# Performance work log

Hardware: AMD Instinct MI355X
Metric: run time of the kernel (lower is better)

Reference implementation:

```python
import jax, jax.numpy as jnp
import numpy as np

N_NODES = 50000
N_EDGES = 800000
D = 64        # in_channels == out_channels
EDGE_DIM = 32
H = 8         # num_heads
HD = D // H   # head_dim


def _layer_norm(x, g, b, eps=1e-5):
    m = jnp.mean(x, axis=-1, keepdims=True)
    v = jnp.mean((x - m) ** 2, axis=-1, keepdims=True)
    return (x - m) * jax.lax.rsqrt(v + eps) * g + b


def setup_inputs() -> dict:
    key = jax.random.key(0)
    ks = jax.random.split(key, 20)
    s = 0.05
    inp = {
        'x': jax.random.normal(ks[0], (N_NODES, D), jnp.float32),
        'edge_index': jax.random.randint(ks[1], (2, N_EDGES), 0, N_NODES, dtype=jnp.int64),
        'edge_attr': jax.random.normal(ks[2], (N_EDGES, EDGE_DIM), jnp.float32),
        'Wq': jax.random.normal(ks[3], (D, D), jnp.float32) * s,
        'bq': jnp.zeros((D,), jnp.float32),
        'Wk': jax.random.normal(ks[4], (D, D), jnp.float32) * s,
        'bk': jnp.zeros((D,), jnp.float32),
        'Wv': jax.random.normal(ks[5], (D, D), jnp.float32) * s,
        'bv': jnp.zeros((D,), jnp.float32),
        'We': jax.random.normal(ks[6], (EDGE_DIM, D), jnp.float32) * s,
        'be': jnp.zeros((D,), jnp.float32),
        'Wo': jax.random.normal(ks[7], (D, D), jnp.float32) * s,
        'bo': jnp.zeros((D,), jnp.float32),
        'g1': jnp.ones((D,), jnp.float32),
        'b1': jnp.zeros((D,), jnp.float32),
        'g2': jnp.ones((D,), jnp.float32),
        'b2': jnp.zeros((D,), jnp.float32),
        'Wf1': jax.random.normal(ks[8], (D, 2 * D), jnp.float32) * s,
        'bf1': jnp.zeros((2 * D,), jnp.float32),
        'Wf2': jax.random.normal(ks[9], (2 * D, D), jnp.float32) * s,
        'bf2': jnp.zeros((D,), jnp.float32),
    }
    return inp


def reference(x, edge_index, edge_attr, Wq, bq, Wk, bk, Wv, bv, We, be, Wo, bo,
              g1, b1, g2, b2, Wf1, bf1, Wf2, bf2):
    num_nodes = x.shape[0]
    # add_self_loops with fill_value=0.0
    ar = jnp.arange(num_nodes, dtype=edge_index.dtype)
    src = jnp.concatenate([edge_index[0], ar])
    dst = jnp.concatenate([edge_index[1], ar])
    ea = jnp.concatenate([edge_attr, jnp.zeros((num_nodes, edge_attr.shape[1]), edge_attr.dtype)])

    q = (x @ Wq + bq).reshape(num_nodes, H, HD)
    k = (x @ Wk + bk).reshape(num_nodes, H, HD)
    v = (x @ Wv + bv).reshape(num_nodes, H, HD)
    ee = (ea @ We + be).reshape(-1, H, HD)  # [E', H, HD]

    # gather, score, global softmax over all edges (dim=0, as in source)
    scores = jnp.sum(q[dst] * (k[src] + ee), axis=-1) / (HD ** 0.5)  # [E', H]
    alpha = jax.nn.softmax(scores, axis=0)
    messages = alpha[..., None] * (v[src] + ee)  # [E', H, HD]

    out_sum = jax.ops.segment_sum(messages, dst, num_segments=num_nodes)
    counts = jax.ops.segment_sum(jnp.ones(dst.shape, x.dtype), dst, num_segments=num_nodes)
    counts = jnp.maximum(counts, 1.0)
    out = (out_sum / counts[:, None, None]).reshape(num_nodes, -1)

    h = _layer_norm(x + out @ Wo + bo, g1, b1)
    ffn = jax.nn.gelu(h @ Wf1 + bf1, approximate=False) @ Wf2 + bf2
    # dropout in eval mode -> identity
    return _layer_norm(h + ffn, g2, b2)
```

## Files before the change

kernel.cpp:

```cpp
#include <hip/hip_runtime.h>
#include <hip/hip_bf16.h>
#include <math.h>

#define N_NODES 50000
#define N_EDGES 800000
#define D 64
#define ED 32

#define Q_OFF    0
#define K_OFF    1600000
#define V_OFF    3200000
#define EE_OFF   4800000
#define OS_OFF   17600000
#define S_OFF    19200000
#define RP_OFF   19200016
#define SRCP_OFF 19250018
#define EIDP_OFF 20050018
#define DEG_OFF  20850018
#define WOFF_OFF 20900018
#define BSUM_OFF 20950018
#define H_OFF    0
#define F1_OFF   EE_OFF

typedef __bf16 bf16x8 __attribute__((ext_vector_type(8)));
typedef float  f32x4  __attribute__((ext_vector_type(4)));

__device__ __forceinline__ ushort f2bf(float f) {
  uint u = __float_as_uint(f);
  uint r = (u + 0x7FFFu + ((u >> 16) & 1u)) >> 16;
  return (ushort)r;
}
__device__ __forceinline__ float bfu2f(ushort u) {
  return __uint_as_float(((uint)u) << 16);
}
__device__ __forceinline__ void unpack8(uint4 u, float (&f)[8]) {
  f[0] = __uint_as_float(u.x << 16); f[1] = __uint_as_float(u.x & 0xffff0000u);
  f[2] = __uint_as_float(u.y << 16); f[3] = __uint_as_float(u.y & 0xffff0000u);
  f[4] = __uint_as_float(u.z << 16); f[5] = __uint_as_float(u.z & 0xffff0000u);
  f[6] = __uint_as_float(u.w << 16); f[7] = __uint_as_float(u.w & 0xffff0000u);
}
__device__ __forceinline__ bf16x8 pack_bf8(float4 a, float4 b) {
  bf16x8 r;
  r[0] = (__bf16)a.x; r[1] = (__bf16)a.y; r[2] = (__bf16)a.z; r[3] = (__bf16)a.w;
  r[4] = (__bf16)b.x; r[5] = (__bf16)b.y; r[6] = (__bf16)b.z; r[7] = (__bf16)b.w;
  return r;
}

__global__ __launch_bounds__(256) void k_qkv_mfma(
    const float* __restrict__ x,
    const float* __restrict__ Wq, const float* __restrict__ bq,
    const float* __restrict__ Wk, const float* __restrict__ bk,
    const float* __restrict__ Wv, const float* __restrict__ bv,
    ushort* __restrict__ q, ushort* __restrict__ k, ushort* __restrict__ v,
    int* __restrict__ deg, float* __restrict__ S) {
  const int tid0 = blockIdx.x * 256 + threadIdx.x;
  if (tid0 < N_NODES) deg[tid0] = 0;
  if (tid0 < 16) S[tid0] = 0.f;

  const int lane = threadIdx.x & 63;
  const int wid  = threadIdx.x >> 6;
  const int r  = lane & 15;
  const int kg = lane >> 4;
  const float* Ws[3] = {Wq, Wk, Wv};
  const float* bs[3] = {bq, bk, bv};
  ushort* os[3] = {q, k, v};

  bf16x8 afrag[3][4][2];
  float  bias[3][4][4];
#pragma unroll
  for (int m = 0; m < 3; ++m)
#pragma unroll
    for (int nt = 0; nt < 4; ++nt) {
#pragma unroll
      for (int kk = 0; kk < 2; ++kk)
#pragma unroll
        for (int j = 0; j < 8; ++j)
          afrag[m][nt][kk][j] = (__bf16)Ws[m][(kk * 32 + kg * 8 + j) * 64 + nt * 16 + r];
#pragma unroll
      for (int j = 0; j < 4; ++j) bias[m][nt][j] = bs[m][nt * 16 + kg * 4 + j];
    }

  const int ntile = N_NODES / 16;
  const int nw = gridDim.x * 4;
  for (int t = blockIdx.x * 4 + wid; t < ntile; t += nw) {
    const int base = t * 16;
    const float4* xr = reinterpret_cast<const float4*>(x + (size_t)(base + r) * 64 + kg * 8);
    const bf16x8 xf0 = pack_bf8(xr[0], xr[1]);
    const bf16x8 xf1 = pack_bf8(xr[8], xr[9]);
#pragma unroll
    for (int m = 0; m < 3; ++m) {
#pragma unroll
      for (int nt = 0; nt < 4; ++nt) {
        f32x4 acc = {bias[m][nt][0], bias[m][nt][1], bias[m][nt][2], bias[m][nt][3]};
        acc = __builtin_amdgcn_mfma_f32_16x16x32_bf16(afrag[m][nt][0], xf0, acc, 0, 0, 0);
        acc = __builtin_amdgcn_mfma_f32_16x16x32_bf16(afrag[m][nt][1], xf1, acc, 0, 0, 0);
        ushort4 pk;
        pk.x = f2bf(acc[0]); pk.y = f2bf(acc[1]); pk.z = f2bf(acc[2]); pk.w = f2bf(acc[3]);
        *reinterpret_cast<ushort4*>(os[m] + (size_t)(base + r) * 64 + nt * 16 + kg * 4) = pk;
      }
    }
  }
}

__global__ __launch_bounds__(256) void k_hist(const int* __restrict__ edst,
                                              int* __restrict__ deg) {
  const int i = blockIdx.x * 256 + threadIdx.x;
  if (i < N_EDGES) atomicAdd(&deg[edst[i]], 1);
}

__global__ __launch_bounds__(256) void k_scan_a(const int* __restrict__ deg,
                                                int* __restrict__ bsum) {
  __shared__ int lds[256];
  const int i = blockIdx.x * 256 + threadIdx.x;
  lds[threadIdx.x] = (i < N_NODES) ? deg[i] : 0;
  __syncthreads();
  for (int s = 128; s > 0; s >>= 1) {
    if (threadIdx.x < s) lds[threadIdx.x] += lds[threadIdx.x + s];
    __syncthreads();
  }
  if (threadIdx.x == 0) bsum[blockIdx.x] = lds[0];
}

__global__ __launch_bounds__(256) void k_scan_b(int* __restrict__ bsum, int nb) {
  __shared__ int lds[256];
  const int t = threadIdx.x;
  const int d = (t < nb) ? bsum[t] : 0;
  lds[t] = d;
  __syncthreads();
  for (int off = 1; off < 256; off <<= 1) {
    const int val = (t >= off) ? lds[t - off] : 0;
    __syncthreads();
    lds[t] += val;
    __syncthreads();
  }
  if (t < nb) bsum[t] = lds[t] - d;
}

__global__ __launch_bounds__(256) void k_scan_c(const int* __restrict__ deg,
                                                const int* __restrict__ bsum,
                                                int* __restrict__ rowptr,
                                                int* __restrict__ woff) {
  __shared__ int lds[256];
  const int i = blockIdx.x * 256 + threadIdx.x;
  const int d = (i < N_NODES) ? deg[i] : 0;
  lds[threadIdx.x] = d;
  __syncthreads();
  for (int off = 1; off < 256; off <<= 1) {
    const int val = (threadIdx.x >= off) ? lds[threadIdx.x - off] : 0;
    __syncthreads();
    lds[threadIdx.x] += val;
    __syncthreads();
  }
  const int ex = bsum[blockIdx.x] + lds[threadIdx.x] - d;
  if (i < N_NODES) { rowptr[i] = ex; woff[i] = ex; }
  if (i == N_NODES - 1) rowptr[N_NODES] = ex + d;
}

__global__ __launch_bounds__(256) void k_scatter(const int* __restrict__ esrc,
                                                 const int* __restrict__ edst,
                                                 int* __restrict__ woff,
                                                 int* __restrict__ srcp,
                                                 int* __restrict__ eidp) {
  const int i = blockIdx.x * 256 + threadIdx.x;
  if (i < N_EDGES) {
    const int pos = atomicAdd(&woff[edst[i]], 1);
    srcp[pos] = esrc[i];
    eidp[pos] = i;
  }
}

__global__ __launch_bounds__(256) void k_ee_mfma(
    const int* __restrict__ eidp, const float* __restrict__ ea,
    const float* __restrict__ We, const float* __restrict__ be,
    unsigned char* __restrict__ ee8) {
  const int lane = threadIdx.x & 63;
  const int wid  = threadIdx.x >> 6;
  const int r  = lane & 15;
  const int kg = lane >> 4;

  bf16x8 afrag[4];
  float  bias[4][4];
#pragma unroll
  for (int nt = 0; nt < 4; ++nt) {
#pragma unroll
    for (int j = 0; j < 8; ++j)
      afrag[nt][j] = (__bf16)We[(kg * 8 + j) * 64 + nt * 16 + r];
#pragma unroll
    for (int j = 0; j < 4; ++j) bias[nt][j] = be[nt * 16 + kg * 4 + j];
  }

  const int ntile = N_EDGES / 16;
  const int nw = gridDim.x * 4;
  for (int t = blockIdx.x * 4 + wid; t < ntile; t += nw) {
    const int base = t * 16;
    const int eid = eidp[base + r];
    const float4* ar = reinterpret_cast<const float4*>(ea + (size_t)eid * 32 + kg * 8);
    const bf16x8 bfrag = pack_bf8(ar[0], ar[1]);
#pragma unroll
    for (int nt = 0; nt < 4; ++nt) {
      f32x4 acc = {bias[nt][0], bias[nt][1], bias[nt][2], bias[nt][3]};
      acc = __builtin_amdgcn_mfma_f32_16x16x32_bf16(afrag[nt], bfrag, acc, 0, 0, 0);
      uint rr = (uint)__builtin_amdgcn_cvt_pk_fp8_f32(acc[0], acc[1], 0, false);
      rr = (uint)__builtin_amdgcn_cvt_pk_fp8_f32(acc[2], acc[3], (int)rr, true);
      *reinterpret_cast<uint*>(ee8 + (size_t)(base + r) * 64 + nt * 16 + kg * 4) = rr;
    }
  }
}

__global__ __launch_bounds__(256) void k_gather(
    const int* __restrict__ rowptr, const int* __restrict__ srcp,
    const unsigned char* __restrict__ ee8,
    const ushort* __restrict__ qb, const ushort* __restrict__ kb,
    const ushort* __restrict__ vb, const float* __restrict__ be,
    ushort* __restrict__ osum, float* __restrict__ S) {
  const int lane = threadIdx.x & 63;
  const int wid  = threadIdx.x >> 6;
  const int h = lane & 7, ei = lane >> 3;
  float bes[8];
#pragma unroll
  for (int i = 0; i < 8; ++i) bes[i] = be[h * 8 + i];
  float sacc = 0.f;
  const int nw = gridDim.x * 4;
  for (int n = blockIdx.x * 4 + wid; n < N_NODES; n += nw) {
    const int beg = rowptr[n], end = rowptr[n + 1];
    float qv[8];
    unpack8(*reinterpret_cast<const uint4*>(qb + (size_t)n * 64 + h * 8), qv);
    float macc[8];
#pragma unroll
    for (int i = 0; i < 8; ++i) macc[i] = 0.f;
    if (ei == 0) {
      float kv[8], vv[8];
      unpack8(*reinterpret_cast<const uint4*>(kb + (size_t)n * 64 + h * 8), kv);
      unpack8(*reinterpret_cast<const uint4*>(vb + (size_t)n * 64 + h * 8), vv);
      float sc = 0.f;
#pragma unroll
      for (int i = 0; i < 8; ++i) sc = fmaf(qv[i], kv[i] + bes[i], sc);
      const float w = __expf(sc * 0.3535533905932738f);
      sacc += w;
#pragma unroll
      for (int i = 0; i < 8; ++i) macc[i] = w * (vv[i] + bes[i]);
    }
    int p = beg + ei;
    int src = (p < end) ? srcp[p] : 0;
    for (; p < end; p += 8) {
      const int nsrc = (p + 8 < end) ? srcp[p + 8] : 0;
      float ev[8], kv[8], vv[8];
      const uint2 er8 = *reinterpret_cast<const uint2*>(ee8 + (size_t)p * 64 + h * 8);
      ev[0] = __builtin_amdgcn_cvt_f32_fp8((int)er8.x, 0);
      ev[1] = __builtin_amdgcn_cvt_f32_fp8((int)er8.x, 1);
      ev[2] = __builtin_amdgcn_cvt_f32_fp8((int)er8.x, 2);
      ev[3] = __builtin_amdgcn_cvt_f32_fp8((int)er8.x, 3);
      ev[4] = __builtin_amdgcn_cvt_f32_fp8((int)er8.y, 0);
      ev[5] = __builtin_amdgcn_cvt_f32_fp8((int)er8.y, 1);
      ev[6] = __builtin_amdgcn_cvt_f32_fp8((int)er8.y, 2);
      ev[7] = __builtin_amdgcn_cvt_f32_fp8((int)er8.y, 3);
      unpack8(*reinterpret_cast<const uint4*>(kb + (size_t)src * 64 + h * 8), kv);
      unpack8(*reinterpret_cast<const uint4*>(vb + (size_t)src * 64 + h * 8), vv);
      float sc = 0.f;
#pragma unroll
      for (int i = 0; i < 8; ++i) sc = fmaf(qv[i], kv[i] + ev[i], sc);
      const float w = __expf(sc * 0.3535533905932738f);
      sacc += w;
#pragma unroll
      for (int i = 0; i < 8; ++i) macc[i] = fmaf(w, vv[i] + ev[i], macc[i]);
      src = nsrc;
    }
#pragma unroll
    for (int i = 0; i < 8; ++i) {
      macc[i] += __shfl_xor(macc[i], 8);
      macc[i] += __shfl_xor(macc[i], 16);
      macc[i] += __shfl_xor(macc[i], 32);
    }
    if (ei == 0) {
      uint pk[4];
#pragma unroll
      for (int i = 0; i < 4; ++i)
        pk[i] = (uint)f2bf(macc[2 * i]) | ((uint)f2bf(macc[2 * i + 1]) << 16);
      *reinterpret_cast<uint4*>(osum + (size_t)n * 64 + h * 8) =
          make_uint4(pk[0], pk[1], pk[2], pk[3]);
    }
  }
  sacc += __shfl_xor(sacc, 8);
  sacc += __shfl_xor(sacc, 16);
  sacc += __shfl_xor(sacc, 32);
  if (ei == 0) atomicAdd(&S[h], sacc);
}

__global__ __launch_bounds__(256) void k_ln1_mfma(
    const ushort* __restrict__ osum, const int* __restrict__ rowptr,
    const float* __restrict__ S, const float* __restrict__ x,
    const float* __restrict__ Wo, const float* __restrict__ bo,
    const float* __restrict__ g1, const float* __restrict__ b1,
    ushort* __restrict__ h) {
  const int lane = threadIdx.x & 63;
  const int wid  = threadIdx.x >> 6;
  const int r  = lane & 15;
  const int kg = lane >> 4;

  bf16x8 afrag[4][2];
  float bias[4][4], g1f[4][4], b1f[4][4];
#pragma unroll
  for (int nt = 0; nt < 4; ++nt) {
#pragma unroll
    for (int kk = 0; kk < 2; ++kk)
#pragma unroll
      for (int j = 0; j < 8; ++j)
        afrag[nt][kk][j] = (__bf16)Wo[(kk * 32 + kg * 8 + j) * 64 + nt * 16 + r];
#pragma unroll
    for (int j = 0; j < 4; ++j) {
      bias[nt][j] = bo[nt * 16 + kg * 4 + j];
      g1f[nt][j]  = g1[nt * 16 + kg * 4 + j];
      b1f[nt][j]  = b1[nt * 16 + kg * 4 + j];
    }
  }
  float invSv[8];
#pragma unroll
  for (int i = 0; i < 8; ++i) invSv[i] = 1.0f / S[i];

  const int ntile = N_NODES / 16;
  const int nw = gridDim.x * 4;
  for (int t = blockIdx.x * 4 + wid; t < ntile; t += nw) {
    const int node = t * 16 + r;
    const float invc = 1.0f / (float)(rowptr[node + 1] - rowptr[node] + 1);
    bf16x8 bfrag[2];
#pragma unroll
    for (int kk = 0; kk < 2; ++kk) {
      float tmp[8];
      unpack8(*reinterpret_cast<const uint4*>(osum + (size_t)node * 64 + kk * 32 + kg * 8), tmp);
      const float sc = invSv[kk * 4 + kg] * invc;
      bf16x8 bf;
#pragma unroll
      for (int e = 0; e < 8; ++e) bf[e] = (__bf16)(tmp[e] * sc);
      bfrag[kk] = bf;
    }
    float tv[4][4];
    float sum = 0.f;
#pragma unroll
    for (int nt = 0; nt < 4; ++nt) {
      f32x4 acc = {bias[nt][0], bias[nt][1], bias[nt][2], bias[nt][3]};
      acc = __builtin_amdgcn_mfma_f32_16x16x32_bf16(afrag[nt][0], bfrag[0], acc, 0, 0, 0);
      acc = __builtin_amdgcn_mfma_f32_16x16x32_bf16(afrag[nt][1], bfrag[1], acc, 0, 0, 0);
      const float4 xv = *reinterpret_cast<const float4*>(x + (size_t)node * 64 + nt * 16 + kg * 4);
      tv[nt][0] = acc[0] + xv.x; tv[nt][1] = acc[1] + xv.y;
      tv[nt][2] = acc[2] + xv.z; tv[nt][3] = acc[3] + xv.w;
      sum += (tv[nt][0] + tv[nt][1]) + (tv[nt][2] + tv[nt][3]);
    }
    sum += __shfl_xor(sum, 16);
    sum += __shfl_xor(sum, 32);
    const float m = sum * (1.0f / 64.0f);
    float var = 0.f;
#pragma unroll
    for (int nt = 0; nt < 4; ++nt)
#pragma unroll
      for (int j = 0; j < 4; ++j) { const float d = tv[nt][j] - m; var = fmaf(d, d, var); }
    var += __shfl_xor(var, 16);
    var += __shfl_xor(var, 32);
    const float rinv = rsqrtf(var * (1.0f / 64.0f) + 1e-5f);
#pragma unroll
    for (int nt = 0; nt < 4; ++nt) {
      ushort4 pk;
      pk.x = f2bf((tv[nt][0] - m) * rinv * g1f[nt][0] + b1f[nt][0]);
      pk.y = f2bf((tv[nt][1] - m) * rinv * g1f[nt][1] + b1f[nt][1]);
      pk.z = f2bf((tv[nt][2] - m) * rinv * g1f[nt][2] + b1f[nt][2]);
      pk.w = f2bf((tv[nt][3] - m) * rinv * g1f[nt][3] + b1f[nt][3]);
      *reinterpret_cast<ushort4*>(h + (size_t)node * 64 + nt * 16 + kg * 4) = pk;
    }
  }
}

__global__ __launch_bounds__(256) void k_ffn1_mfma(
    const ushort* __restrict__ h, const float* __restrict__ Wf1,
    const float* __restrict__ bf1, ushort* __restrict__ f1) {
  const int lane = threadIdx.x & 63;
  const int wid  = threadIdx.x >> 6;
  const int r  = lane & 15;
  const int kg = lane >> 4;

  bf16x8 afrag[8][2];
  float bias[8][4];
#pragma unroll
  for (int nt = 0; nt < 8; ++nt) {
#pragma unroll
    for (int kk = 0; kk < 2; ++kk)
#pragma unroll
      for (int j = 0; j < 8; ++j)
        afrag[nt][kk][j] = (__bf16)Wf1[(kk * 32 + kg * 8 + j) * 128 + nt * 16 + r];
#pragma unroll
    for (int j = 0; j < 4; ++j) bias[nt][j] = bf1[nt * 16 + kg * 4 + j];
  }

  const int ntile = N_NODES / 16;
  const int nw = gridDim.x * 4;
  for (int t = blockIdx.x * 4 + wid; t < ntile; t += nw) {
    const int node = t * 16 + r;
    const bf16x8 bf0 = *reinterpret_cast<const bf16x8*>(h + (size_t)node * 64 + kg * 8);
    const bf16x8 bf1g = *reinterpret_cast<const bf16x8*>(h + (size_t)node * 64 + 32 + kg * 8);
#pragma unroll
    for (int nt = 0; nt < 8; ++nt) {
      f32x4 acc = {bias[nt][0], bias[nt][1], bias[nt][2], bias[nt][3]};
      acc = __builtin_amdgcn_mfma_f32_16x16x32_bf16(afrag[nt][0], bf0, acc, 0, 0, 0);
      acc = __builtin_amdgcn_mfma_f32_16x16x32_bf16(afrag[nt][1], bf1g, acc, 0, 0, 0);
      ushort4 pk;
      pk.x = f2bf(0.5f * acc[0] * (1.0f + erff(acc[0] * 0.7071067811865475f)));
      pk.y = f2bf(0.5f * acc[1] * (1.0f + erff(acc[1] * 0.7071067811865475f)));
      pk.z = f2bf(0.5f * acc[2] * (1.0f + erff(acc[2] * 0.7071067811865475f)));
      pk.w = f2bf(0.5f * acc[3] * (1.0f + erff(acc[3] * 0.7071067811865475f)));
      *reinterpret_cast<ushort4*>(f1 + (size_t)node * 128 + nt * 16 + kg * 4) = pk;
    }
  }
}

__global__ __launch_bounds__(256) void k_ffn2_mfma(
    const ushort* __restrict__ f1, const ushort* __restrict__ h,
    const float* __restrict__ Wf2, const float* __restrict__ bf2,
    const float* __restrict__ g2, const float* __restrict__ b2,
    float* __restrict__ out) {
  const int lane = threadIdx.x & 63;
  const int wid  = threadIdx.x >> 6;
  const int r  = lane & 15;
  const int kg = lane >> 4;

  bf16x8 afrag[4][4];
  float bias[4][4], g2f[4][4], b2f[4][4];
#pragma unroll
  for (int nt = 0; nt < 4; ++nt) {
#pragma unroll
    for (int kk = 0; kk < 4; ++kk)
#pragma unroll
      for (int j = 0; j < 8; ++j)
        afrag[nt][kk][j] = (__bf16)Wf2[(kk * 32 + kg * 8 + j) * 64 + nt * 16 + r];
#pragma unroll
    for (int j = 0; j < 4; ++j) {
      bias[nt][j] = bf2[nt * 16 + kg * 4 + j];
      g2f[nt][j]  = g2[nt * 16 + kg * 4 + j];
      b2f[nt][j]  = b2[nt * 16 + kg * 4 + j];
    }
  }

  const int ntile = N_NODES / 16;
  const int nw = gridDim.x * 4;
  for (int t = blockIdx.x * 4 + wid; t < ntile; t += nw) {
    const int node = t * 16 + r;
    bf16x8 bfrag[4];
#pragma unroll
    for (int kk = 0; kk < 4; ++kk)
      bfrag[kk] = *reinterpret_cast<const bf16x8*>(f1 + (size_t)node * 128 + kk * 32 + kg * 8);
    float tv[4][4];
    float sum = 0.f;
#pragma unroll
    for (int nt = 0; nt < 4; ++nt) {
      f32x4 acc = {bias[nt][0], bias[nt][1], bias[nt][2], bias[nt][3]};
      acc = __builtin_amdgcn_mfma_f32_16x16x32_bf16(afrag[nt][0], bfrag[0], acc, 0, 0, 0);
      acc = __builtin_amdgcn_mfma_f32_16x16x32_bf16(afrag[nt][1], bfrag[1], acc, 0, 0, 0);
      acc = __builtin_amdgcn_mfma_f32_16x16x32_bf16(afrag[nt][2], bfrag[2], acc, 0, 0, 0);
      acc = __builtin_amdgcn_mfma_f32_16x16x32_bf16(afrag[nt][3], bfrag[3], acc, 0, 0, 0);
      const ushort4 hv = *reinterpret_cast<const ushort4*>(h + (size_t)node * 64 + nt * 16 + kg * 4);
      tv[nt][0] = acc[0] + bfu2f(hv.x); tv[nt][1] = acc[1] + bfu2f(hv.y);
      tv[nt][2] = acc[2] + bfu2f(hv.z); tv[nt][3] = acc[3] + bfu2f(hv.w);
      sum += (tv[nt][0] + tv[nt][1]) + (tv[nt][2] + tv[nt][3]);
    }
    sum += __shfl_xor(sum, 16);
    sum += __shfl_xor(sum, 32);
    const float m = sum * (1.0f / 64.0f);
    float var = 0.f;
#pragma unroll
    for (int nt = 0; nt < 4; ++nt)
#pragma unroll
      for (int j = 0; j < 4; ++j) { const float d = tv[nt][j] - m; var = fmaf(d, d, var); }
    var += __shfl_xor(var, 16);
    var += __shfl_xor(var, 32);
    const float rinv = rsqrtf(var * (1.0f / 64.0f) + 1e-5f);
#pragma unroll
    for (int nt = 0; nt < 4; ++nt) {
      float4 o;
      o.x = (tv[nt][0] - m) * rinv * g2f[nt][0] + b2f[nt][0];
      o.y = (tv[nt][1] - m) * rinv * g2f[nt][1] + b2f[nt][1];
      o.z = (tv[nt][2] - m) * rinv * g2f[nt][2] + b2f[nt][2];
      o.w = (tv[nt][3] - m) * rinv * g2f[nt][3] + b2f[nt][3];
      *reinterpret_cast<float4*>(out + (size_t)node * 64 + nt * 16 + kg * 4) = o;
    }
  }
}

extern "C" void kernel_launch(void* const* d_in, const int* in_sizes, int n_in,
                              void* d_out, int out_size, void* d_ws, size_t ws_size,
                              hipStream_t stream) {
  const float* x    = (const float*)d_in[0];
  const int*   ei   = (const int*)d_in[1];
  const int*   esrc = ei;
  const int*   edst = ei + N_EDGES;
  const float* ea   = (const float*)d_in[2];
  const float* Wq   = (const float*)d_in[3];
  const float* bq   = (const float*)d_in[4];
  const float* Wk   = (const float*)d_in[5];
  const float* bk   = (const float*)d_in[6];
  const float* Wv   = (const float*)d_in[7];
  const float* bv   = (const float*)d_in[8];
  const float* We   = (const float*)d_in[9];
  const float* be   = (const float*)d_in[10];
  const float* Wo   = (const float*)d_in[11];
  const float* bo   = (const float*)d_in[12];
  const float* g1   = (const float*)d_in[13];
  const float* b1   = (const float*)d_in[14];
  const float* g2   = (const float*)d_in[15];
  const float* b2   = (const float*)d_in[16];
  const float* Wf1  = (const float*)d_in[17];
  const float* bf1  = (const float*)d_in[18];
  const float* Wf2  = (const float*)d_in[19];
  const float* bf2  = (const float*)d_in[20];

  float* ws    = (float*)d_ws;
  ushort* q    = (ushort*)(ws + Q_OFF);
  ushort* k    = (ushort*)(ws + K_OFF);
  ushort* v    = (ushort*)(ws + V_OFF);
  unsigned char* ee8 = (unsigned char*)(ws + EE_OFF);
  ushort* osum = (ushort*)(ws + OS_OFF);
  float* S     = ws + S_OFF;
  int*   rowptr = (int*)(ws + RP_OFF);
  int*   srcp   = (int*)(ws + SRCP_OFF);
  int*   eidp   = (int*)(ws + EIDP_OFF);
  int*   deg    = (int*)(ws + DEG_OFF);
  int*   woff   = (int*)(ws + WOFF_OFF);
  int*   bsum   = (int*)(ws + BSUM_OFF);
  ushort* h    = (ushort*)(ws + H_OFF);
  ushort* f1   = (ushort*)(ws + F1_OFF);
  float* out   = (float*)d_out;

  const dim3 B(256);
  const int nodeBlocks = (N_NODES + 255) / 256;
  const int edgeBlocks = (N_EDGES + 255) / 256;

  k_qkv_mfma<<<dim3(256), B, 0, stream>>>(x, Wq, bq, Wk, bk, Wv, bv, q, k, v, deg, S);
  k_hist<<<dim3(edgeBlocks), B, 0, stream>>>(edst, deg);
  k_scan_a<<<dim3(nodeBlocks), B, 0, stream>>>(deg, bsum);
  k_scan_b<<<dim3(1), B, 0, stream>>>(bsum, nodeBlocks);
  k_scan_c<<<dim3(nodeBlocks), B, 0, stream>>>(deg, bsum, rowptr, woff);
  k_scatter<<<dim3(edgeBlocks), B, 0, stream>>>(esrc, edst, woff, srcp, eidp);
  k_ee_mfma<<<dim3(1024), B, 0, stream>>>(eidp, ea, We, be, ee8);
  k_gather<<<dim3(1024), B, 0, stream>>>(rowptr, srcp, ee8, q, k, v, be, osum, S);
  k_ln1_mfma<<<dim3(256), B, 0, stream>>>(osum, rowptr, S, x, Wo, bo, g1, b1, h);
  k_ffn1_mfma<<<dim3(256), B, 0, stream>>>(h, Wf1, bf1, f1);
  k_ffn2_mfma<<<dim3(256), B, 0, stream>>>(f1, h, Wf2, bf2, g2, b2, out);
}
```

Measured before the change: 262.5 us.

## Fuse histogram into QKV kernel, merge scan stages, prefetch gather loads

The degree histogram is folded into the QKV projection kernel through a grid-stride atomic loop, and deg is now zeroed by a memset instead of inside that kernel. The three-pass scan becomes two passes: each block reduces the preceding block sums itself rather than relying on a separate single-block scan. The gather loop software-pipelines the next edge's ee, k and v loads one iteration ahead, not just the source index. Together these cut kernel launches and hide gather latency, at the cost of more registers in the gather kernel and redundant block-sum reductions.

```diff
diff --git a/kernel.cpp b/kernel.cpp
--- a/kernel.cpp
+++ b/kernel.cpp
@@ -6,6 +6,7 @@
 #define N_EDGES 800000
 #define D 64
 #define ED 32
+#define NB 196
 
 #define Q_OFF    0
 #define K_OFF    1600000
@@ -52,9 +53,9 @@
     const float* __restrict__ Wk, const float* __restrict__ bk,
     const float* __restrict__ Wv, const float* __restrict__ bv,
     ushort* __restrict__ q, ushort* __restrict__ k, ushort* __restrict__ v,
-    int* __restrict__ deg, float* __restrict__ S) {
+    const int* __restrict__ edst, int* __restrict__ deg,
+    float* __restrict__ S) {
   const int tid0 = blockIdx.x * 256 + threadIdx.x;
-  if (tid0 < N_NODES) deg[tid0] = 0;
   if (tid0 < 16) S[tid0] = 0.f;
 
   const int lane = threadIdx.x & 63;
@@ -100,12 +101,9 @@
       }
     }
   }
-}
-
-__global__ __launch_bounds__(256) void k_hist(const int* __restrict__ edst,
-                                              int* __restrict__ deg) {
-  const int i = blockIdx.x * 256 + threadIdx.x;
-  if (i < N_EDGES) atomicAdd(&deg[edst[i]], 1);
+
+  const int stride = gridDim.x * 256;
+  for (int i = tid0; i < N_EDGES; i += stride) atomicAdd(&deg[edst[i]], 1);
 }
 
 __global__ __launch_bounds__(256) void k_scan_a(const int* __restrict__ deg,
@@ -121,10 +119,22 @@
   if (threadIdx.x == 0) bsum[blockIdx.x] = lds[0];
 }
 
-__global__ __launch_bounds__(256) void k_scan_b(int* __restrict__ bsum, int nb) {
+__global__ __launch_bounds__(256) void k_scan_c(const int* __restrict__ deg,
+                                                const int* __restrict__ bsum,
+                                                int* __restrict__ rowptr,
+                                                int* __restrict__ woff) {
   __shared__ int lds[256];
   const int t = threadIdx.x;
-  const int d = (t < nb) ? bsum[t] : 0;
+  lds[t] = (t < blockIdx.x) ? bsum[t] : 0;
+  __syncthreads();
+  for (int s = 128; s > 0; s >>= 1) {
+    if (t < s) lds[t] += lds[t + s];
+    __syncthreads();
+  }
+  const int base0 = lds[0];
+  __syncthreads();
+  const int i = blockIdx.x * 256 + t;
+  const int d = (i < N_NODES) ? deg[i] : 0;
   lds[t] = d;
   __syncthreads();
   for (int off = 1; off < 256; off <<= 1) {
@@ -133,25 +143,7 @@
     lds[t] += val;
     __syncthreads();
   }
-  if (t < nb) bsum[t] = lds[t] - d;
-}
-
-__global__ __launch_bounds__(256) void k_scan_c(const int* __restrict__ deg,
-                                                const int* __restrict__ bsum,
-                                                int* __restrict__ rowptr,
-                                                int* __restrict__ woff) {
-  __shared__ int lds[256];
-  const int i = blockIdx.x * 256 + threadIdx.x;
-  const int d = (i < N_NODES) ? deg[i] : 0;
-  lds[threadIdx.x] = d;
-  __syncthreads();
-  for (int off = 1; off < 256; off <<= 1) {
-    const int val = (threadIdx.x >= off) ? lds[threadIdx.x - off] : 0;
-    __syncthreads();
-    lds[threadIdx.x] += val;
-    __syncthreads();
-  }
-  const int ex = bsum[blockIdx.x] + lds[threadIdx.x] - d;
+  const int ex = base0 + lds[t] - d;
   if (i < N_NODES) { rowptr[i] = ex; woff[i] = ex; }
   if (i == N_NODES - 1) rowptr[N_NODES] = ex + d;
 }
@@ -241,21 +233,35 @@
       for (int i = 0; i < 8; ++i) macc[i] = w * (vv[i] + bes[i]);
     }
     int p = beg + ei;
-    int src = (p < end) ? srcp[p] : 0;
+    uint2 ecur = make_uint2(0u, 0u);
+    uint4 kcur = make_uint4(0u, 0u, 0u, 0u), vcur = make_uint4(0u, 0u, 0u, 0u);
+    if (p < end) {
+      const int s0 = srcp[p];
+      ecur = *reinterpret_cast<const uint2*>(ee8 + (size_t)p * 64 + h * 8);
+      kcur = *reinterpret_cast<const uint4*>(kb + (size_t)s0 * 64 + h * 8);
+      vcur = *reinterpret_cast<const uint4*>(vb + (size_t)s0 * 64 + h * 8);
+    }
     for (; p < end; p += 8) {
-      const int nsrc = (p + 8 < end) ? srcp[p + 8] : 0;
+      uint2 enx = make_uint2(0u, 0u);
+      uint4 knx = make_uint4(0u, 0u, 0u, 0u), vnx = make_uint4(0u, 0u, 0u, 0u);
+      const int pn = p + 8;
+      if (pn < end) {
+        const int sn = srcp[pn];
+        enx = *reinterpret_cast<const uint2*>(ee8 + (size_t)pn * 64 + h * 8);
+        knx = *reinterpret_cast<const uint4*>(kb + (size_t)sn * 64 + h * 8);
+        vnx = *reinterpret_cast<const uint4*>(vb + (size_t)sn * 64 + h * 8);
+      }
       float ev[8], kv[8], vv[8];
-      const uint2 er8 = *reinterpret_cast<const uint2*>(ee8 + (size_t)p * 64 + h * 8);
-      ev[0] = __builtin_amdgcn_cvt_f32_fp8((int)er8.x, 0);
-      ev[1] = __builtin_amdgcn_cvt_f32_fp8((int)er8.x, 1);
-      ev[2] = __builtin_amdgcn_cvt_f32_fp8((int)er8.x, 2);
-      ev[3] = __builtin_amdgcn_cvt_f32_fp8((int)er8.x, 3);
-      ev[4] = __builtin_amdgcn_cvt_f32_fp8((int)er8.y, 0);
-      ev[5] = __builtin_amdgcn_cvt_f32_fp8((int)er8.y, 1);
-      ev[6] = __builtin_amdgcn_cvt_f32_fp8((int)er8.y, 2);
-      ev[7] = __builtin_amdgcn_cvt_f32_fp8((int)er8.y, 3);
-      unpack8(*reinterpret_cast<const uint4*>(kb + (size_t)src * 64 + h * 8), kv);
-      unpack8(*reinterpret_cast<const uint4*>(vb + (size_t)src * 64 + h * 8), vv);
+      ev[0] = __builtin_amdgcn_cvt_f32_fp8((int)ecur.x, 0);
+      ev[1] = __builtin_amdgcn_cvt_f32_fp8((int)ecur.x, 1);
+      ev[2] = __builtin_amdgcn_cvt_f32_fp8((int)ecur.x, 2);
+      ev[3] = __builtin_amdgcn_cvt_f32_fp8((int)ecur.x, 3);
+      ev[4] = __builtin_amdgcn_cvt_f32_fp8((int)ecur.y, 0);
+      ev[5] = __builtin_amdgcn_cvt_f32_fp8((int)ecur.y, 1);
+      ev[6] = __builtin_amdgcn_cvt_f32_fp8((int)ecur.y, 2);
+      ev[7] = __builtin_amdgcn_cvt_f32_fp8((int)ecur.y, 3);
+      unpack8(kcur, kv);
+      unpack8(vcur, vv);
       float sc = 0.f;
 #pragma unroll
       for (int i = 0; i < 8; ++i) sc = fmaf(qv[i], kv[i] + ev[i], sc);
@@ -263,7 +269,7 @@
       sacc += w;
 #pragma unroll
       for (int i = 0; i < 8; ++i) macc[i] = fmaf(w, vv[i] + ev[i], macc[i]);
-      src = nsrc;
+      ecur = enx; kcur = knx; vcur = vnx;
     }
 #pragma unroll
     for (int i = 0; i < 8; ++i) {
@@ -527,14 +533,12 @@
   float* out   = (float*)d_out;
 
   const dim3 B(256);
-  const int nodeBlocks = (N_NODES + 255) / 256;
   const int edgeBlocks = (N_EDGES + 255) / 256;
 
-  k_qkv_mfma<<<dim3(256), B, 0, stream>>>(x, Wq, bq, Wk, bk, Wv, bv, q, k, v, deg, S);
-  k_hist<<<dim3(edgeBlocks), B, 0, stream>>>(edst, deg);
-  k_scan_a<<<dim3(nodeBlocks), B, 0, stream>>>(deg, bsum);
-  k_scan_b<<<dim3(1), B, 0, stream>>>(bsum, nodeBlocks);
-  k_scan_c<<<dim3(nodeBlocks), B, 0, stream>>>(deg, bsum, rowptr, woff);
+  hipMemsetAsync(deg, 0, (size_t)N_NODES * sizeof(int), stream);
+  k_qkv_mfma<<<dim3(256), B, 0, stream>>>(x, Wq, bq, Wk, bk, Wv, bv, q, k, v, edst, deg, S);
+  k_scan_a<<<dim3(NB), B, 0, stream>>>(deg, bsum);
+  k_scan_c<<<dim3(NB), B, 0, stream>>>(deg, bsum, rowptr, woff);
   k_scatter<<<dim3(edgeBlocks), B, 0, stream>>>(esrc, edst, woff, srcp, eidp);
   k_ee_mfma<<<dim3(1024), B, 0, stream>>>(eidp, ea, We, be, ee8);
   k_gather<<<dim3(1024), B, 0, stream>>>(rowptr, srcp, ee8, q, k, v, be, osum, S);
```

New measurement: 268.0 us. +2.1%, slower.

## Store K/V in fp8, merge scan kernels, and scatter edge embeddings by position

Applied to the files above, without the earlier changes.

K and V projections are now stored as fp8 instead of bf16. This halves the bytes gathered per edge in the attention kernel, which is memory-bound on random source lookups. The two-level scan drops its single-block middle kernel: each block now reduces the preceding block sums itself, saving one launch. The edge embedding kernel reads edge_attr contiguously and writes to the CSR position through a per-edge pos array, instead of gathering edge_attr by a permuted id. fp8 K/V lowers precision, which risks accuracy.

```diff
diff --git a/kernel.cpp b/kernel.cpp
--- a/kernel.cpp
+++ b/kernel.cpp
@@ -6,19 +6,20 @@
 #define N_EDGES 800000
 #define D 64
 #define ED 32
+#define NB 196
 
 #define Q_OFF    0
-#define K_OFF    1600000
-#define V_OFF    3200000
-#define EE_OFF   4800000
-#define OS_OFF   17600000
-#define S_OFF    19200000
-#define RP_OFF   19200016
-#define SRCP_OFF 19250018
-#define EIDP_OFF 20050018
-#define DEG_OFF  20850018
-#define WOFF_OFF 20900018
-#define BSUM_OFF 20950018
+#define K8_OFF   1600000
+#define V8_OFF   2400000
+#define EE_OFF   3200000
+#define OS_OFF   16000000
+#define S_OFF    17600000
+#define RP_OFF   17600016
+#define SRCP_OFF 17650018
+#define POSE_OFF 18450018
+#define DEG_OFF  19250018
+#define WOFF_OFF 19300018
+#define BSUM_OFF 19350018
 #define H_OFF    0
 #define F1_OFF   EE_OFF
 
@@ -39,19 +40,34 @@
   f[4] = __uint_as_float(u.z << 16); f[5] = __uint_as_float(u.z & 0xffff0000u);
   f[6] = __uint_as_float(u.w << 16); f[7] = __uint_as_float(u.w & 0xffff0000u);
 }
+__device__ __forceinline__ void unfp8(uint2 u, float (&f)[8]) {
+  f[0] = __builtin_amdgcn_cvt_f32_fp8((int)u.x, 0);
+  f[1] = __builtin_amdgcn_cvt_f32_fp8((int)u.x, 1);
+  f[2] = __builtin_amdgcn_cvt_f32_fp8((int)u.x, 2);
+  f[3] = __builtin_amdgcn_cvt_f32_fp8((int)u.x, 3);
+  f[4] = __builtin_amdgcn_cvt_f32_fp8((int)u.y, 0);
+  f[5] = __builtin_amdgcn_cvt_f32_fp8((int)u.y, 1);
+  f[6] = __builtin_amdgcn_cvt_f32_fp8((int)u.y, 2);
+  f[7] = __builtin_amdgcn_cvt_f32_fp8((int)u.y, 3);
+}
 __device__ __forceinline__ bf16x8 pack_bf8(float4 a, float4 b) {
   bf16x8 r;
   r[0] = (__bf16)a.x; r[1] = (__bf16)a.y; r[2] = (__bf16)a.z; r[3] = (__bf16)a.w;
   r[4] = (__bf16)b.x; r[5] = (__bf16)b.y; r[6] = (__bf16)b.z; r[7] = (__bf16)b.w;
   return r;
 }
+__device__ __forceinline__ uint pk_fp8(f32x4 acc) {
+  uint rr = (uint)__builtin_amdgcn_cvt_pk_fp8_f32(acc[0], acc[1], 0, false);
+  return (uint)__builtin_amdgcn_cvt_pk_fp8_f32(acc[2], acc[3], (int)rr, true);
+}
 
 __global__ __launch_bounds__(256) void k_qkv_mfma(
     const float* __restrict__ x,
     const float* __restrict__ Wq, const float* __restrict__ bq,
     const float* __restrict__ Wk, const float* __restrict__ bk,
     const float* __restrict__ Wv, const float* __restrict__ bv,
-    ushort* __restrict__ q, ushort* __restrict__ k, ushort* __restrict__ v,
+    ushort* __restrict__ q, unsigned char* __restrict__ k8,
+    unsigned char* __restrict__ v8,
     int* __restrict__ deg, float* __restrict__ S) {
   const int tid0 = blockIdx.x * 256 + threadIdx.x;
   if (tid0 < N_NODES) deg[tid0] = 0;
@@ -63,7 +79,6 @@
   const int kg = lane >> 4;
   const float* Ws[3] = {Wq, Wk, Wv};
   const float* bs[3] = {bq, bk, bv};
-  ushort* os[3] = {q, k, v};
 
   bf16x8 afrag[3][4][2];
   float  bias[3][4][4];
@@ -94,9 +109,14 @@
         f32x4 acc = {bias[m][nt][0], bias[m][nt][1], bias[m][nt][2], bias[m][nt][3]};
         acc = __builtin_amdgcn_mfma_f32_16x16x32_bf16(afrag[m][nt][0], xf0, acc, 0, 0, 0);
         acc = __builtin_amdgcn_mfma_f32_16x16x32_bf16(afrag[m][nt][1], xf1, acc, 0, 0, 0);
-        ushort4 pk;
-        pk.x = f2bf(acc[0]); pk.y = f2bf(acc[1]); pk.z = f2bf(acc[2]); pk.w = f2bf(acc[3]);
-        *reinterpret_cast<ushort4*>(os[m] + (size_t)(base + r) * 64 + nt * 16 + kg * 4) = pk;
+        if (m == 0) {
+          ushort4 pk;
+          pk.x = f2bf(acc[0]); pk.y = f2bf(acc[1]); pk.z = f2bf(acc[2]); pk.w = f2bf(acc[3]);
+          *reinterpret_cast<ushort4*>(q + (size_t)(base + r) * 64 + nt * 16 + kg * 4) = pk;
+        } else {
+          unsigned char* dst = (m == 1) ? k8 : v8;
+          *reinterpret_cast<uint*>(dst + (size_t)(base + r) * 64 + nt * 16 + kg * 4) = pk_fp8(acc);
+        }
       }
     }
   }
@@ -121,10 +141,22 @@
   if (threadIdx.x == 0) bsum[blockIdx.x] = lds[0];
 }
 
-__global__ __launch_bounds__(256) void k_scan_b(int* __restrict__ bsum, int nb) {
+__global__ __launch_bounds__(256) void k_scan_c(const int* __restrict__ deg,
+                                                const int* __restrict__ bsum,
+                                                int* __restrict__ rowptr,
+                                                int* __restrict__ woff) {
   __shared__ int lds[256];
   const int t = threadIdx.x;
-  const int d = (t < nb) ? bsum[t] : 0;
+  lds[t] = (t < blockIdx.x) ? bsum[t] : 0;
+  __syncthreads();
+  for (int s = 128; s > 0; s >>= 1) {
+    if (t < s) lds[t] += lds[t + s];
+    __syncthreads();
+  }
+  const int base0 = lds[0];
+  __syncthreads();
+  const int i = blockIdx.x * 256 + t;
+  const int d = (i < N_NODES) ? deg[i] : 0;
   lds[t] = d;
   __syncthreads();
   for (int off = 1; off < 256; off <<= 1) {
@@ -133,25 +165,7 @@
     lds[t] += val;
     __syncthreads();
   }
-  if (t < nb) bsum[t] = lds[t] - d;
-}
-
-__global__ __launch_bounds__(256) void k_scan_c(const int* __restrict__ deg,
-                                                const int* __restrict__ bsum,
-                                                int* __restrict__ rowptr,
-                                                int* __restrict__ woff) {
-  __shared__ int lds[256];
-  const int i = blockIdx.x * 256 + threadIdx.x;
-  const int d = (i < N_NODES) ? deg[i] : 0;
-  lds[threadIdx.x] = d;
-  __syncthreads();
-  for (int off = 1; off < 256; off <<= 1) {
-    const int val = (threadIdx.x >= off) ? lds[threadIdx.x - off] : 0;
-    __syncthreads();
-    lds[threadIdx.x] += val;
-    __syncthreads();
-  }
-  const int ex = bsum[blockIdx.x] + lds[threadIdx.x] - d;
+  const int ex = base0 + lds[t] - d;
   if (i < N_NODES) { rowptr[i] = ex; woff[i] = ex; }
   if (i == N_NODES - 1) rowptr[N_NODES] = ex + d;
 }
@@ -160,17 +174,17 @@
                                                  const int* __restrict__ edst,
                                                  int* __restrict__ woff,
                                                  int* __restrict__ srcp,
-                                                 int* __restrict__ eidp) {
+                                                 int* __restrict__ pose) {
   const int i = blockIdx.x * 256 + threadIdx.x;
   if (i < N_EDGES) {
     const int pos = atomicAdd(&woff[edst[i]], 1);
     srcp[pos] = esrc[i];
-    eidp[pos] = i;
+    pose[i] = pos;
   }
 }
 
 __global__ __launch_bounds__(256) void k_ee_mfma(
-    const int* __restrict__ eidp, const float* __restrict__ ea,
+    const int* __restrict__ pose, const float* __restrict__ ea,
     const float* __restrict__ We, const float* __restrict__ be,
     unsigned char* __restrict__ ee8) {
   const int lane = threadIdx.x & 63;
@@ -193,16 +207,14 @@
   const int nw = gridDim.x * 4;
   for (int t = blockIdx.x * 4 + wid; t < ntile; t += nw) {
     const int base = t * 16;
-    const int eid = eidp[base + r];
-    const float4* ar = reinterpret_cast<const float4*>(ea + (size_t)eid * 32 + kg * 8);
+    const int pos = pose[base + r];
+    const float4* ar = reinterpret_cast<const float4*>(ea + (size_t)(base + r) * 32 + kg * 8);
     const bf16x8 bfrag = pack_bf8(ar[0], ar[1]);
 #pragma unroll
     for (int nt = 0; nt < 4; ++nt) {
       f32x4 acc = {bias[nt][0], bias[nt][1], bias[nt][2], bias[nt][3]};
       acc = __builtin_amdgcn_mfma_f32_16x16x32_bf16(afrag[nt], bfrag, acc, 0, 0, 0);
-      uint rr = (uint)__builtin_amdgcn_cvt_pk_fp8_f32(acc[0], acc[1], 0, false);
-      rr = (uint)__builtin_amdgcn_cvt_pk_fp8_f32(acc[2], acc[3], (int)rr, true);
-      *reinterpret_cast<uint*>(ee8 + (size_t)(base + r) * 64 + nt * 16 + kg * 4) = rr;
+      *reinterpret_cast<uint*>(ee8 + (size_t)pos * 64 + nt * 16 + kg * 4) = pk_fp8(acc);
     }
   }
 }
@@ -210,8 +222,8 @@
 __global__ __launch_bounds__(256) void k_gather(
     const int* __restrict__ rowptr, const int* __restrict__ srcp,
     const unsigned char* __restrict__ ee8,
-    const ushort* __restrict__ qb, const ushort* __restrict__ kb,
-    const ushort* __restrict__ vb, const float* __restrict__ be,
+    const ushort* __restrict__ qb, const unsigned char* __restrict__ k8,
+    const unsigned char* __restrict__ v8, const float* __restrict__ be,
     ushort* __restrict__ osum, float* __restrict__ S) {
   const int lane = threadIdx.x & 63;
   const int wid  = threadIdx.x >> 6;
@@ -230,8 +242,8 @@
     for (int i = 0; i < 8; ++i) macc[i] = 0.f;
     if (ei == 0) {
       float kv[8], vv[8];
-      unpack8(*reinterpret_cast<const uint4*>(kb + (size_t)n * 64 + h * 8), kv);
-      unpack8(*reinterpret_cast<const uint4*>(vb + (size_t)n * 64 + h * 8), vv);
+      unfp8(*reinterpret_cast<const uint2*>(k8 + (size_t)n * 64 + h * 8), kv);
+      unfp8(*reinterpret_cast<const uint2*>(v8 + (size_t)n * 64 + h * 8), vv);
       float sc = 0.f;
 #pragma unroll
       for (int i = 0; i < 8; ++i) sc = fmaf(qv[i], kv[i] + bes[i], sc);
@@ -245,17 +257,9 @@
     for (; p < end; p += 8) {
       const int nsrc = (p + 8 < end) ? srcp[p + 8] : 0;
       float ev[8], kv[8], vv[8];
-      const uint2 er8 = *reinterpret_cast<const uint2*>(ee8 + (size_t)p * 64 + h * 8);
-      ev[0] = __builtin_amdgcn_cvt_f32_fp8((int)er8.x, 0);
-      ev[1] = __builtin_amdgcn_cvt_f32_fp8((int)er8.x, 1);
-      ev[2] = __builtin_amdgcn_cvt_f32_fp8((int)er8.x, 2);
-      ev[3] = __builtin_amdgcn_cvt_f32_fp8((int)er8.x, 3);
-      ev[4] = __builtin_amdgcn_cvt_f32_fp8((int)er8.y, 0);
-      ev[5] = __builtin_amdgcn_cvt_f32_fp8((int)er8.y, 1);
-      ev[6] = __builtin_amdgcn_cvt_f32_fp8((int)er8.y, 2);
-      ev[7] = __builtin_amdgcn_cvt_f32_fp8((int)er8.y, 3);
-      unpack8(*reinterpret_cast<const uint4*>(kb + (size_t)src * 64 + h * 8), kv);
-      unpack8(*reinterpret_cast<const uint4*>(vb + (size_t)src * 64 + h * 8), vv);
+      unfp8(*reinterpret_cast<const uint2*>(ee8 + (size_t)p * 64 + h * 8), ev);
+      unfp8(*reinterpret_cast<const uint2*>(k8 + (size_t)src * 64 + h * 8), kv);
+      unfp8(*reinterpret_cast<const uint2*>(v8 + (size_t)src * 64 + h * 8), vv);
       float sc = 0.f;
 #pragma unroll
       for (int i = 0; i < 8; ++i) sc = fmaf(qv[i], kv[i] + ev[i], sc);
@@ -511,14 +515,14 @@
 
   float* ws    = (float*)d_ws;
   ushort* q    = (ushort*)(ws + Q_OFF);
-  ushort* k    = (ushort*)(ws + K_OFF);
-  ushort* v    = (ushort*)(ws + V_OFF);
+  unsigned char* k8  = (unsigned char*)(ws + K8_OFF);
+  unsigned char* v8  = (unsigned char*)(ws + V8_OFF);
   unsigned char* ee8 = (unsigned char*)(ws + EE_OFF);
   ushort* osum = (ushort*)(ws + OS_OFF);
   float* S     = ws + S_OFF;
   int*   rowptr = (int*)(ws + RP_OFF);
   int*   srcp   = (int*)(ws + SRCP_OFF);
-  int*   eidp   = (int*)(ws + EIDP_OFF);
+  int*   pose   = (int*)(ws + POSE_OFF);
   int*   deg    = (int*)(ws + DEG_OFF);
   int*   woff   = (int*)(ws + WOFF_OFF);
   int*   bsum   = (int*)(ws + BSUM_OFF);
@@ -527,17 +531,15 @@
   float* out   = (float*)d_out;
 
   const dim3 B(256);
-  const int nodeBlocks = (N_NODES + 255) / 256;
   const int edgeBlocks = (N_EDGES + 255) / 256;
 
-  k_qkv_mfma<<<dim3(256), B, 0, stream>>>(x, Wq, bq, Wk, bk, Wv, bv, q, k, v, deg, S);
+  k_qkv_mfma<<<dim3(256), B, 0, stream>>>(x, Wq, bq, Wk, bk, Wv, bv, q, k8, v8, deg, S);
   k_hist<<<dim3(edgeBlocks), B, 0, stream>>>(edst, deg);
-  k_scan_a<<<dim3(nodeBlocks), B, 0, stream>>>(deg, bsum);
-  k_scan_b<<<dim3(1), B, 0, stream>>>(bsum, nodeBlocks);
-  k_scan_c<<<dim3(nodeBlocks), B, 0, stream>>>(deg, bsum, rowptr, woff);
-  k_scatter<<<dim3(edgeBlocks), B, 0, stream>>>(esrc, edst, woff, srcp, eidp);
-  k_ee_mfma<<<dim3(1024), B, 0, stream>>>(eidp, ea, We, be, ee8);
-  k_gather<<<dim3(1024), B, 0, stream>>>(rowptr, srcp, ee8, q, k, v, be, osum, S);
+  k_scan_a<<<dim3(NB), B, 0, stream>>>(deg, bsum);
+  k_scan_c<<<dim3(NB), B, 0, stream>>>(deg, bsum, rowptr, woff);
+  k_scatter<<<dim3(edgeBlocks), B, 0, stream>>>(esrc, edst, woff, srcp, pose);
+  k_ee_mfma<<<dim3(1024), B, 0, stream>>>(pose, ea, We, be, ee8);
+  k_gather<<<dim3(1024), B, 0, stream>>>(rowptr, srcp, ee8, q, k8, v8, be, osum, S);
   k_ln1_mfma<<<dim3(256), B, 0, stream>>>(osum, rowptr, S, x, Wo, bo, g1, b1, h);
   k_ffn1_mfma<<<dim3(256), B, 0, stream>>>(h, Wf1, bf1, f1);
   k_ffn2_mfma<<<dim3(256), B, 0, stream>>>(f1, h, Wf2, bf2, g2, b2, out);
```

Result: slower. 269.0 us (+2.5%).
